# Optimization experiments

Measured on AMD Instinct MI355X. Metric: run time of the kernel, lower is better.

## Reference

```python
import jax, jax.numpy as jnp
import numpy as np
import math

D_MODEL = 2048
N_HEADS = 16
D_HEAD = D_MODEL // N_HEADS  # 128, also the RoPE dim
ROPE_BASE = 10000.0
B, T = 2, 2048


def _rope_cos_sin(seq_len, dim, dtype):
    inv_freq = 1.0 / (ROPE_BASE ** (jnp.arange(0, dim, 2, dtype=jnp.float32) / dim))
    t = jnp.arange(seq_len, dtype=jnp.float32)
    freqs = jnp.einsum('i,j->ij', t, inv_freq)          # [T, dim/2]
    emb = jnp.concatenate((freqs, freqs), axis=-1)       # [T, dim]  (half-concat layout, as in source)
    cos = jnp.cos(emb)[None, None, :, :].astype(dtype)   # [1,1,T,dim]
    sin = jnp.sin(emb)[None, None, :, :].astype(dtype)
    return cos, sin


def _apply_rot(x, cos, sin, dim):
    # interleaved pair rotation, faithful to the torch code
    x1 = x[..., 0:dim:2]
    x2 = x[..., 1:dim:2]
    x_rot = jnp.stack((-x2, x1), axis=-1).reshape(x.shape[:-1] + (dim,))
    return x[..., :dim] * cos + x_rot * sin


def setup_inputs() -> dict:
    key = jax.random.key(0)
    k1, k2, k3 = jax.random.split(key, 3)
    x = jax.random.normal(k1, (B, T, D_MODEL), dtype=jnp.float32)
    # causal additive mask, broadcastable to [B,H,T,T]
    neg = jnp.finfo(jnp.float32).min / 2
    causal = jnp.triu(jnp.full((T, T), neg, dtype=jnp.float32), k=1)
    mask = causal[None, None, :, :]
    Wqkv = jax.random.normal(k2, (D_MODEL, 3 * D_MODEL), dtype=jnp.float32) * (1.0 / math.sqrt(D_MODEL))
    bqkv = jnp.zeros((3 * D_MODEL,), dtype=jnp.float32)
    Wo = jax.random.normal(k3, (D_MODEL, D_MODEL), dtype=jnp.float32) * (1.0 / math.sqrt(D_MODEL))
    bo = jnp.zeros((D_MODEL,), dtype=jnp.float32)
    return {"x": x, "mask": mask, "Wqkv": Wqkv, "bqkv": bqkv, "Wo": Wo, "bo": bo}


def reference(x, mask, Wqkv, bqkv, Wo, bo):
    Bx, Tx, C = x.shape
    qkv = x @ Wqkv + bqkv                                     # [B,T,3C]
    qkv = qkv.reshape(Bx, Tx, 3, N_HEADS, D_HEAD)
    qkv = jnp.transpose(qkv, (2, 0, 3, 1, 4))                 # [3,B,H,T,dh]
    q, k, v = qkv[0], qkv[1], qkv[2]
    cos, sin = _rope_cos_sin(Tx, D_HEAD, x.dtype)
    q = _apply_rot(q, cos, sin, D_HEAD)
    k = _apply_rot(k, cos, sin, D_HEAD)
    att = jnp.einsum('bhqd,bhkd->bhqk', q, k) / math.sqrt(D_HEAD)
    att = att + mask
    att = jax.nn.softmax(att, axis=-1)
    y = jnp.einsum('bhqk,bhkd->bhqd', att, v)                 # [B,H,T,dh]
    y = jnp.transpose(y, (0, 2, 1, 3)).reshape(Bx, Tx, C)
    return y @ Wo + bo
```

## Files before the change

kernel.cpp:

```cpp
#include <hip/hip_runtime.h>
#include <stdint.h>

#define TDIM 2048
#define DMODEL 2048
#define NHEADS 16
#define DHEAD 128
#define NBATCH 2
#define NTOK (NBATCH * TDIM)
#define NQKV (3 * DMODEL)
#define BHTOT (NBATCH * NHEADS)

typedef unsigned short u16;
typedef __attribute__((ext_vector_type(8))) short bf16x8;
typedef __attribute__((ext_vector_type(4))) float f32x4;
typedef __attribute__((ext_vector_type(4))) int i32x4;

__device__ __forceinline__ u16 f2bf(float f) {
  union { float f; uint32_t u; } v; v.f = f;
  uint32_t u = v.u + 0x7fffu + ((v.u >> 16) & 1u);
  return (u16)(u >> 16);
}
__device__ __forceinline__ float bf2f(u16 h) {
  union { uint32_t u; float f; } v; v.u = ((uint32_t)h) << 16;
  return v.f;
}

#define GLOAD16(g, l)                                                        \
  __builtin_amdgcn_global_load_lds(                                          \
      (const __attribute__((address_space(1))) void*)(g),                    \
      (__attribute__((address_space(3))) void*)(l), 16, 0, 0)

__global__ void rope_table_kernel(float* __restrict__ ct, float* __restrict__ st) {
  int idx = blockIdx.x * 256 + threadIdx.x;
  int t = idx >> 6, m = idx & 63;
  float inv = expf(-(float)m * (9.210340371976184f / 64.0f));
  float ang = (float)t * inv;
  ct[idx] = cosf(ang);
  st[idx] = sinf(ang);
}

__global__ void convert_kernel(const float* __restrict__ in, u16* __restrict__ out) {
  int i = blockIdx.x * 256 + threadIdx.x;
  float4 v = ((const float4*)in)[i];
  ushort4 o;
  o.x = f2bf(v.x); o.y = f2bf(v.y); o.z = f2bf(v.z); o.w = f2bf(v.w);
  ((ushort4*)out)[i] = o;
}

__global__ __launch_bounds__(256) void transpose_convert_kernel(
    const float* __restrict__ in, u16* __restrict__ out, int K, int N) {
  __shared__ u16 tile[32][33];
  int n0 = blockIdx.x * 32, k0 = blockIdx.y * 32;
  int tx = threadIdx.x, ty = threadIdx.y;
  #pragma unroll
  for (int q = 0; q < 4; q++) {
    int k = ty + q * 8;
    tile[k][tx] = f2bf(in[(size_t)(k0 + k) * N + n0 + tx]);
  }
  __syncthreads();
  #pragma unroll
  for (int q = 0; q < 4; q++) {
    int n = ty + q * 8;
    out[(size_t)(n0 + n) * K + k0 + tx] = tile[tx][n];
  }
}

__global__ __launch_bounds__(256) void vtrans_kernel(
    const u16* __restrict__ Vtmp, u16* __restrict__ Vt) {
  __shared__ u16 tile[32][33];
  int bh = blockIdx.z;
  int t0 = blockIdx.x * 32, d0 = blockIdx.y * 32;
  int tx = threadIdx.x, ty = threadIdx.y;
  const u16* src = Vtmp + (size_t)bh * TDIM * DHEAD;
  u16* dst = Vt + (size_t)bh * DHEAD * TDIM;
  #pragma unroll
  for (int q = 0; q < 4; q++) {
    int t = ty + q * 8;
    tile[t][tx] = src[(size_t)(t0 + t) * DHEAD + d0 + tx];
  }
  __syncthreads();
  #pragma unroll
  for (int q = 0; q < 4; q++) {
    int d = ty + q * 8;
    dst[(size_t)(d0 + d) * TDIM + t0 + tx] = tile[tx][d];
  }
}

__global__ void rope_kernel(u16* __restrict__ X, const float* __restrict__ ct,
                            const float* __restrict__ st, float scale) {
  int idx = blockIdx.x * 256 + threadIdx.x;
  int i = idx & 63;
  int t = (idx >> 6) & (TDIM - 1);
  size_t base = (size_t)idx * 2;
  float x0 = bf2f(X[base]), x1 = bf2f(X[base + 1]);
  int j0 = (2 * i) & 63, j1 = (2 * i + 1) & 63;
  const float* ctt = ct + (size_t)t * 64;
  const float* stt = st + (size_t)t * 64;
  float c0 = ctt[j0], s0 = stt[j0], c1 = ctt[j1], s1 = stt[j1];
  X[base]     = f2bf((x0 * c0 - x1 * s0) * scale);
  X[base + 1] = f2bf((x1 * c1 + x0 * s1) * scale);
}

template <int MODE>
__global__ __launch_bounds__(512, 2) void gemm_bt_kernel(
    const u16* __restrict__ A, const u16* __restrict__ Bt,
    const float* __restrict__ bias,
    u16* __restrict__ q_out, u16* __restrict__ k_out, u16* __restrict__ v_out,
    float* __restrict__ f_out, int K) {
  __shared__ __attribute__((aligned(128))) char lds[2][49152];
  const int tid = threadIdx.x;
  const int lane = tid & 63, w = tid >> 6;
  const int wr = w >> 2, wc = w & 3;
  const int g = lane >> 4, c = lane & 15;
  const int m0 = blockIdx.x * 128, n0 = blockIdx.y * 256;
  const size_t rowb = (size_t)K * 2;
  const int NKT = K >> 6;

  const char* aSrc[2]; int aDst[2];
  const char* bSrc[4]; int bDst[4];
  #pragma unroll
  for (int p = 0; p < 2; p++) {
    int o = p * 8192 + tid * 16;
    int row = o >> 7, j = (o >> 4) & 7;
    aSrc[p] = (const char*)A + (size_t)(m0 + row) * rowb + ((j ^ (row & 7)) << 4);
    aDst[p] = o;
  }
  #pragma unroll
  for (int p = 0; p < 4; p++) {
    int o = p * 8192 + tid * 16;
    int row = o >> 7, j = (o >> 4) & 7;
    bSrc[p] = (const char*)Bt + (size_t)(n0 + row) * rowb + ((j ^ (row & 7)) << 4);
    bDst[p] = 16384 + o;
  }

#define STAGE(bufp, kt)                                                      \
  {                                                                          \
    const size_t kb_ = (size_t)(kt) * 128;                                   \
    _Pragma("unroll") for (int p_ = 0; p_ < 2; p_++)                         \
        GLOAD16(aSrc[p_] + kb_, (bufp) + aDst[p_]);                          \
    _Pragma("unroll") for (int p_ = 0; p_ < 4; p_++)                         \
        GLOAD16(bSrc[p_] + kb_, (bufp) + bDst[p_]);                          \
  }

  int aRd[4][2], bRd[4][2];
  #pragma unroll
  for (int m = 0; m < 4; m++) {
    #pragma unroll
    for (int ks = 0; ks < 2; ks++) {
      int arow = wr * 64 + m * 16 + c;
      aRd[m][ks] = arow * 128 + (((ks * 4 + g) ^ (c & 7)) << 4);
      int brow = wc * 64 + m * 16 + c;
      bRd[m][ks] = 16384 + brow * 128 + (((ks * 4 + g) ^ (c & 7)) << 4);
    }
  }

  const f32x4 zero = {0.f, 0.f, 0.f, 0.f};
  f32x4 acc[4][4];
  #pragma unroll
  for (int m = 0; m < 4; m++)
    #pragma unroll
    for (int n = 0; n < 4; n++) acc[m][n] = zero;

  STAGE(lds[0], 0);
  STAGE(lds[1], 1);
  asm volatile("s_waitcnt vmcnt(6)" ::: "memory");
  __builtin_amdgcn_s_barrier();
  __builtin_amdgcn_sched_barrier(0);

  int cur = 0;
  for (int kt = 0; kt < NKT; kt++) {
    char* bp = cur ? lds[1] : lds[0];
    bf16x8 bfr[4][2], afr[2][2], af2[2][2];
    #pragma unroll
    for (int n = 0; n < 4; n++)
      #pragma unroll
      for (int ks = 0; ks < 2; ks++)
        bfr[n][ks] = *(const bf16x8*)(bp + bRd[n][ks]);
    #pragma unroll
    for (int m = 0; m < 2; m++)
      #pragma unroll
      for (int ks = 0; ks < 2; ks++)
        afr[m][ks] = *(const bf16x8*)(bp + aRd[m][ks]);
    __builtin_amdgcn_s_setprio(1);
    #pragma unroll
    for (int ks = 0; ks < 2; ks++)
      #pragma unroll
      for (int m = 0; m < 2; m++)
        #pragma unroll
        for (int n = 0; n < 4; n++)
          acc[m][n] = __builtin_amdgcn_mfma_f32_16x16x32_bf16(
              afr[m][ks], bfr[n][ks], acc[m][n], 0, 0, 0);
    __builtin_amdgcn_s_setprio(0);

    #pragma unroll
    for (int m = 0; m < 2; m++)
      #pragma unroll
      for (int ks = 0; ks < 2; ks++)
        af2[m][ks] = *(const bf16x8*)(bp + aRd[m + 2][ks]);
    asm volatile("s_waitcnt lgkmcnt(0)" ::: "memory");
    __builtin_amdgcn_s_barrier();
    __builtin_amdgcn_sched_barrier(0);
    if (kt + 2 < NKT) STAGE(bp, kt + 2);
    __builtin_amdgcn_s_setprio(1);
    #pragma unroll
    for (int ks = 0; ks < 2; ks++)
      #pragma unroll
      for (int m = 0; m < 2; m++)
        #pragma unroll
        for (int n = 0; n < 4; n++)
          acc[m + 2][n] = __builtin_amdgcn_mfma_f32_16x16x32_bf16(
              af2[m][ks], bfr[n][ks], acc[m + 2][n], 0, 0, 0);
    __builtin_amdgcn_s_setprio(0);

    if (kt < NKT - 1) {
      if (kt + 2 < NKT) {
        asm volatile("s_waitcnt vmcnt(6)" ::: "memory");
      } else {
        asm volatile("s_waitcnt vmcnt(0)" ::: "memory");
      }
      __builtin_amdgcn_s_barrier();
      __builtin_amdgcn_sched_barrier(0);
    }
    cur ^= 1;
  }
#undef STAGE

  #pragma unroll
  for (int m = 0; m < 4; m++) {
    #pragma unroll
    for (int n = 0; n < 4; n++) {
      int gcol = n0 + wc * 64 + n * 16 + c;
      float bv = bias[gcol];
      #pragma unroll
      for (int r = 0; r < 4; r++) {
        int grow = m0 + wr * 64 + m * 16 + g * 4 + r;
        float val = acc[m][n][r] + bv;
        if (MODE == 0) {
          int s = gcol >> 11;
          int rem = gcol & 2047;
          int h = rem >> 7, d = rem & 127;
          int b = grow >> 11, t = grow & (TDIM - 1);
          size_t off = (((size_t)(b * NHEADS + h)) * TDIM + t) * DHEAD + d;
          u16 hv = f2bf(val);
          if (s == 0) q_out[off] = hv;
          else if (s == 1) k_out[off] = hv;
          else v_out[off] = hv;
        } else {
          f_out[(size_t)grow * DMODEL + gcol] = val;
        }
      }
    }
  }
}

__global__ __launch_bounds__(256) void attn_kernel(
    const u16* __restrict__ Q, const u16* __restrict__ K,
    const u16* __restrict__ Vt, u16* __restrict__ Yattn) {
  __shared__ u16 Ks[2][64 * 128];
  __shared__ u16 Vs[2][128 * 64];
  __shared__ u16 Ps[4][16 * 64];
  const int tid = threadIdx.x, lane = tid & 63, w = tid >> 6;
  const int g = lane >> 4, c = lane & 15;
  const int bh = blockIdx.y, b = bh >> 4, h = bh & 15;
  const u16* Qp = Q + (size_t)bh * TDIM * DHEAD;
  const u16* Kp = K + (size_t)bh * TDIM * DHEAD;
  const u16* Vp = Vt + (size_t)bh * DHEAD * TDIM;
  const f32x4 zero = {0.f, 0.f, 0.f, 0.f};

  for (int half = 0; half < 2; half++) {
    const int qt = half ? (31 - (int)blockIdx.x) : (int)blockIdx.x;
    const int qb = qt * 64 + w * 16;

    bf16x8 qf[4];
    #pragma unroll
    for (int kc = 0; kc < 4; kc++)
      qf[kc] = *(const bf16x8*)(Qp + (size_t)(qb + c) * DHEAD + kc * 32 + g * 8);

    f32x4 po[8];
    #pragma unroll
    for (int df = 0; df < 8; df++) po[df] = zero;
    float mrun[4], lrun[4];
    #pragma unroll
    for (int r = 0; r < 4; r++) { mrun[r] = -1e30f; lrun[r] = 0.f; }

    const int nt = qt + 1;

    {
      #pragma unroll
      for (int p = 0; p < 4; p++) {
        int off = p * 4096 + tid * 16;
        int kr = off >> 8, kc4 = (off & 255) >> 4;
        GLOAD16((const char*)Kp + (size_t)kr * 256 + ((kc4 ^ (kr & 7)) << 4),
                (char*)Ks[0] + off);
        int vr = off >> 7, vc4 = (off & 127) >> 4;
        GLOAD16((const char*)Vp + (size_t)vr * (TDIM * 2) + ((vc4 ^ (vr & 7)) << 4),
                (char*)Vs[0] + off);
      }
    }
    __syncthreads();

    int cur = 0;
    for (int t = 0; t < nt; t++) {
      if (t + 1 < nt) {
        int kv0n = (t + 1) * 64;
        char* KsN = (char*)Ks[cur ^ 1];
        char* VsN = (char*)Vs[cur ^ 1];
        #pragma unroll
        for (int p = 0; p < 4; p++) {
          int off = p * 4096 + tid * 16;
          int kr = off >> 8, kc4 = (off & 255) >> 4;
          GLOAD16((const char*)Kp + (size_t)(kv0n + kr) * 256 +
                      ((kc4 ^ (kr & 7)) << 4),
                  KsN + off);
          int vr = off >> 7, vc4 = (off & 127) >> 4;
          GLOAD16((const char*)Vp + (size_t)vr * (TDIM * 2) + (size_t)kv0n * 2 +
                      ((vc4 ^ (vr & 7)) << 4),
                  VsN + off);
        }
      }

      const u16* KsC = Ks[cur];
      const u16* VsC = Vs[cur];
      const int kv0 = t * 64;

      f32x4 sa[4];
      #pragma unroll
      for (int n = 0; n < 4; n++) sa[n] = zero;
      __builtin_amdgcn_s_setprio(1);
      #pragma unroll
      for (int n = 0; n < 4; n++) {
        int krow = n * 16 + c;
        #pragma unroll
        for (int kc = 0; kc < 4; kc++) {
          int kb = (kc * 32 + g * 8) * 2;
          bf16x8 kf = *(const bf16x8*)((const char*)KsC + krow * 256 +
                                       (kb ^ ((krow & 7) << 4)));
          sa[n] = __builtin_amdgcn_mfma_f32_16x16x32_bf16(qf[kc], kf, sa[n], 0, 0, 0);
        }
      }
      __builtin_amdgcn_s_setprio(0);

      if (kv0 + 63 > qb) {
        #pragma unroll
        for (int n = 0; n < 4; n++) {
          int col = kv0 + n * 16 + c;
          #pragma unroll
          for (int r = 0; r < 4; r++) {
            int qrow = qb + g * 4 + r;
            if (col > qrow) sa[n][r] = -1e30f;
          }
        }
      }

      float pvals[4][4];
      #pragma unroll
      for (int r = 0; r < 4; r++) {
        float vmax = fmaxf(fmaxf(sa[0][r], sa[1][r]), fmaxf(sa[2][r], sa[3][r]));
        #pragma unroll
        for (int d = 1; d < 16; d <<= 1) vmax = fmaxf(vmax, __shfl_xor(vmax, d, 64));
        float mnew = fmaxf(mrun[r], vmax);
        float scale = __expf(mrun[r] - mnew);
        float rs = 0.f;
        #pragma unroll
        for (int n = 0; n < 4; n++) {
          float p = __expf(sa[n][r] - mnew);
          pvals[r][n] = p;
          rs += p;
        }
        #pragma unroll
        for (int d = 1; d < 16; d <<= 1) rs += __shfl_xor(rs, d, 64);
        lrun[r] = lrun[r] * scale + rs;
        mrun[r] = mnew;
        #pragma unroll
        for (int df = 0; df < 8; df++) po[df][r] *= scale;
      }

      char* Pw = (char*)&Ps[w][0];
      #pragma unroll
      for (int r = 0; r < 4; r++) {
        int ri = g * 4 + r;
        #pragma unroll
        for (int n = 0; n < 4; n++) {
          int colb = (n * 16 + c) * 2;
          *(u16*)(Pw + ri * 128 + (colb ^ ((ri & 7) << 4))) = f2bf(pvals[r][n]);
        }
      }
      bf16x8 pa[2];
      #pragma unroll
      for (int kc2 = 0; kc2 < 2; kc2++) {
        int pb = (kc2 * 32 + g * 8) * 2;
        pa[kc2] = *(const bf16x8*)(Pw + c * 128 + (pb ^ ((c & 7) << 4)));
      }
      __builtin_amdgcn_s_setprio(1);
      #pragma unroll
      for (int df = 0; df < 8; df++) {
        #pragma unroll
        for (int kc2 = 0; kc2 < 2; kc2++) {
          int vrow = df * 16 + c;
          int vb = (kc2 * 32 + g * 8) * 2;
          bf16x8 vf = *(const bf16x8*)((const char*)VsC + vrow * 128 +
                                       (vb ^ ((vrow & 7) << 4)));
          po[df] = __builtin_amdgcn_mfma_f32_16x16x32_bf16(pa[kc2], vf, po[df], 0, 0, 0);
        }
      }
      __builtin_amdgcn_s_setprio(0);

      __syncthreads();
      cur ^= 1;
    }

    float inv[4];
    #pragma unroll
    for (int r = 0; r < 4; r++) inv[r] = 1.0f / lrun[r];
    #pragma unroll
    for (int df = 0; df < 8; df++) {
      #pragma unroll
      for (int r = 0; r < 4; r++) {
        int trow = qb + g * 4 + r;
        int col = h * DHEAD + df * 16 + c;
        Yattn[((size_t)b * TDIM + trow) * DMODEL + col] = f2bf(po[df][r] * inv[r]);
      }
    }
  }
}

extern "C" void kernel_launch(void* const* d_in, const int* in_sizes, int n_in,
                              void* d_out, int out_size, void* d_ws, size_t ws_size,
                              hipStream_t stream) {
  const float* x    = (const float*)d_in[0];
  const float* Wqkv = (const float*)d_in[2];
  const float* bqkv = (const float*)d_in[3];
  const float* Wo   = (const float*)d_in[4];
  const float* bo   = (const float*)d_in[5];
  float* out = (float*)d_out;

  char* ws = (char*)d_ws;
  size_t o = 0;
  u16* xb    = (u16*)(ws + o); o += (size_t)NTOK * DMODEL * 2;
  u16* Wqkvt = (u16*)(ws + o); o += (size_t)NQKV * DMODEL * 2;
  u16* Wot   = (u16*)(ws + o); o += (size_t)DMODEL * DMODEL * 2;
  u16* Qb    = (u16*)(ws + o); o += (size_t)BHTOT * TDIM * DHEAD * 2;
  u16* Kb    = (u16*)(ws + o); o += (size_t)BHTOT * TDIM * DHEAD * 2;
  u16* Vtmp  = (u16*)(ws + o); o += (size_t)BHTOT * TDIM * DHEAD * 2;
  float* ct  = (float*)(ws + o); o += (size_t)TDIM * 64 * 4;
  float* st  = (float*)(ws + o); o += (size_t)TDIM * 64 * 4;
  u16* Vt    = xb;
  u16* Yattn = Vtmp;

  dim3 tb32x8(32, 8);

  rope_table_kernel<<<(TDIM * 64) / 256, 256, 0, stream>>>(ct, st);
  convert_kernel<<<(NTOK * DMODEL / 4) / 256, 256, 0, stream>>>(x, xb);
  transpose_convert_kernel<<<dim3(NQKV / 32, DMODEL / 32), tb32x8, 0, stream>>>(
      Wqkv, Wqkvt, DMODEL, NQKV);
  transpose_convert_kernel<<<dim3(DMODEL / 32, DMODEL / 32), tb32x8, 0, stream>>>(
      Wo, Wot, DMODEL, DMODEL);

  gemm_bt_kernel<0><<<dim3(NTOK / 128, NQKV / 256), 512, 0, stream>>>(
      xb, Wqkvt, bqkv, Qb, Kb, Vtmp, nullptr, DMODEL);

  rope_kernel<<<(BHTOT * TDIM * 64) / 256, 256, 0, stream>>>(
      Qb, ct, st, 0.08838834764831845f);
  rope_kernel<<<(BHTOT * TDIM * 64) / 256, 256, 0, stream>>>(Kb, ct, st, 1.0f);

  vtrans_kernel<<<dim3(TDIM / 32, DHEAD / 32, BHTOT), tb32x8, 0, stream>>>(Vtmp, Vt);

  attn_kernel<<<dim3(16, BHTOT), 256, 0, stream>>>(Qb, Kb, Vt, Yattn);

  gemm_bt_kernel<1><<<dim3(NTOK / 128, DMODEL / 256), 512, 0, stream>>>(
      Yattn, Wot, bo, nullptr, nullptr, nullptr, out, DMODEL);
}
```

Before: 305.6 us.

## Fuse RoPE into QKV GEMM epilogue and switch to triple-buffered LDS pipeline

Removes the two standalone RoPE kernels by applying the rotation and the Q scaling in the QKV GEMM epilogue, with a lane shuffle supplying each pair's partner value. This avoids an extra read and write of Q and K. The GEMM main loop also moves from a double-buffered, split-phase schedule to a three-stage LDS ring with one barrier per k-step. That raises LDS per block to 144KB, which likely limits occupancy to one block per CU despite the launch bounds of 2.

```diff
diff --git a/kernel.cpp b/kernel.cpp
--- a/kernel.cpp
+++ b/kernel.cpp
@@ -86,28 +86,14 @@
   }
 }
 
-__global__ void rope_kernel(u16* __restrict__ X, const float* __restrict__ ct,
-                            const float* __restrict__ st, float scale) {
-  int idx = blockIdx.x * 256 + threadIdx.x;
-  int i = idx & 63;
-  int t = (idx >> 6) & (TDIM - 1);
-  size_t base = (size_t)idx * 2;
-  float x0 = bf2f(X[base]), x1 = bf2f(X[base + 1]);
-  int j0 = (2 * i) & 63, j1 = (2 * i + 1) & 63;
-  const float* ctt = ct + (size_t)t * 64;
-  const float* stt = st + (size_t)t * 64;
-  float c0 = ctt[j0], s0 = stt[j0], c1 = ctt[j1], s1 = stt[j1];
-  X[base]     = f2bf((x0 * c0 - x1 * s0) * scale);
-  X[base + 1] = f2bf((x1 * c1 + x0 * s1) * scale);
-}
-
 template <int MODE>
 __global__ __launch_bounds__(512, 2) void gemm_bt_kernel(
     const u16* __restrict__ A, const u16* __restrict__ Bt,
     const float* __restrict__ bias,
     u16* __restrict__ q_out, u16* __restrict__ k_out, u16* __restrict__ v_out,
-    float* __restrict__ f_out, int K) {
-  __shared__ __attribute__((aligned(128))) char lds[2][49152];
+    float* __restrict__ f_out,
+    const float* __restrict__ ct, const float* __restrict__ st, int K) {
+  __shared__ __attribute__((aligned(128))) char lds[3][49152];
   const int tid = threadIdx.x;
   const int lane = tid & 63, w = tid >> 6;
   const int wr = w >> 2, wc = w & 3;
@@ -163,65 +149,42 @@
 
   STAGE(lds[0], 0);
   STAGE(lds[1], 1);
-  asm volatile("s_waitcnt vmcnt(6)" ::: "memory");
-  __builtin_amdgcn_s_barrier();
-  __builtin_amdgcn_sched_barrier(0);
-
-  int cur = 0;
+
   for (int kt = 0; kt < NKT; kt++) {
-    char* bp = cur ? lds[1] : lds[0];
-    bf16x8 bfr[4][2], afr[2][2], af2[2][2];
+    if (kt + 1 < NKT) {
+      asm volatile("s_waitcnt vmcnt(6)" ::: "memory");
+    } else {
+      asm volatile("s_waitcnt vmcnt(0)" ::: "memory");
+    }
+    __builtin_amdgcn_s_barrier();
+    __builtin_amdgcn_sched_barrier(0);
+
+    char* bp = lds[kt % 3];
+    if (kt + 2 < NKT) STAGE(lds[(kt + 2) % 3], kt + 2);
+
+    bf16x8 afr[4][2], bfr[4][2];
     #pragma unroll
     for (int n = 0; n < 4; n++)
       #pragma unroll
       for (int ks = 0; ks < 2; ks++)
         bfr[n][ks] = *(const bf16x8*)(bp + bRd[n][ks]);
     #pragma unroll
-    for (int m = 0; m < 2; m++)
+    for (int m = 0; m < 4; m++)
       #pragma unroll
       for (int ks = 0; ks < 2; ks++)
         afr[m][ks] = *(const bf16x8*)(bp + aRd[m][ks]);
+
     __builtin_amdgcn_s_setprio(1);
     #pragma unroll
     for (int ks = 0; ks < 2; ks++)
       #pragma unroll
-      for (int m = 0; m < 2; m++)
+      for (int m = 0; m < 4; m++)
         #pragma unroll
         for (int n = 0; n < 4; n++)
           acc[m][n] = __builtin_amdgcn_mfma_f32_16x16x32_bf16(
               afr[m][ks], bfr[n][ks], acc[m][n], 0, 0, 0);
     __builtin_amdgcn_s_setprio(0);
-
-    #pragma unroll
-    for (int m = 0; m < 2; m++)
-      #pragma unroll
-      for (int ks = 0; ks < 2; ks++)
-        af2[m][ks] = *(const bf16x8*)(bp + aRd[m + 2][ks]);
-    asm volatile("s_waitcnt lgkmcnt(0)" ::: "memory");
-    __builtin_amdgcn_s_barrier();
     __builtin_amdgcn_sched_barrier(0);
-    if (kt + 2 < NKT) STAGE(bp, kt + 2);
-    __builtin_amdgcn_s_setprio(1);
-    #pragma unroll
-    for (int ks = 0; ks < 2; ks++)
-      #pragma unroll
-      for (int m = 0; m < 2; m++)
-        #pragma unroll
-        for (int n = 0; n < 4; n++)
-          acc[m + 2][n] = __builtin_amdgcn_mfma_f32_16x16x32_bf16(
-              af2[m][ks], bfr[n][ks], acc[m + 2][n], 0, 0, 0);
-    __builtin_amdgcn_s_setprio(0);
-
-    if (kt < NKT - 1) {
-      if (kt + 2 < NKT) {
-        asm volatile("s_waitcnt vmcnt(6)" ::: "memory");
-      } else {
-        asm volatile("s_waitcnt vmcnt(0)" ::: "memory");
-      }
-      __builtin_amdgcn_s_barrier();
-      __builtin_amdgcn_sched_barrier(0);
-    }
-    cur ^= 1;
   }
 #undef STAGE
 
@@ -231,22 +194,40 @@
     for (int n = 0; n < 4; n++) {
       int gcol = n0 + wc * 64 + n * 16 + c;
       float bv = bias[gcol];
-      #pragma unroll
-      for (int r = 0; r < 4; r++) {
-        int grow = m0 + wr * 64 + m * 16 + g * 4 + r;
-        float val = acc[m][n][r] + bv;
-        if (MODE == 0) {
-          int s = gcol >> 11;
-          int rem = gcol & 2047;
-          int h = rem >> 7, d = rem & 127;
-          int b = grow >> 11, t = grow & (TDIM - 1);
-          size_t off = (((size_t)(b * NHEADS + h)) * TDIM + t) * DHEAD + d;
-          u16 hv = f2bf(val);
-          if (s == 0) q_out[off] = hv;
-          else if (s == 1) k_out[off] = hv;
-          else v_out[off] = hv;
+      float val[4];
+      #pragma unroll
+      for (int r = 0; r < 4; r++) val[r] = acc[m][n][r] + bv;
+      if (MODE == 0) {
+        int s = n0 >> 11;
+        int rem = gcol & 2047;
+        int h = rem >> 7, d = rem & 127;
+        int b0 = (m0 + wr * 64 + m * 16) >> 11;
+        size_t hb = (((size_t)(b0 * NHEADS + h)) * TDIM) * DHEAD + d;
+        if (s == 2) {
+          #pragma unroll
+          for (int r = 0; r < 4; r++) {
+            int t = (m0 + wr * 64 + m * 16 + g * 4 + r) & (TDIM - 1);
+            v_out[hb + (size_t)t * DHEAD] = f2bf(val[r]);
+          }
         } else {
-          f_out[(size_t)grow * DMODEL + gcol] = val;
+          int mf = gcol & 63;
+          float sgn = (c & 1) ? 1.0f : -1.0f;
+          u16* dst = (s == 0) ? q_out : k_out;
+          float qs = (s == 0) ? 0.08838834764831845f : 1.0f;
+          #pragma unroll
+          for (int r = 0; r < 4; r++) {
+            float part = __shfl_xor(val[r], 1, 64);
+            int t = (m0 + wr * 64 + m * 16 + g * 4 + r) & (TDIM - 1);
+            float cs = ct[t * 64 + mf], sn = st[t * 64 + mf];
+            float rot = (val[r] * cs + sgn * part * sn) * qs;
+            dst[hb + (size_t)t * DHEAD] = f2bf(rot);
+          }
+        }
+      } else {
+        #pragma unroll
+        for (int r = 0; r < 4; r++) {
+          int grow = m0 + wr * 64 + m * 16 + g * 4 + r;
+          f_out[(size_t)grow * DMODEL + gcol] = val[r];
         }
       }
     }
@@ -457,16 +438,12 @@
       Wo, Wot, DMODEL, DMODEL);
 
   gemm_bt_kernel<0><<<dim3(NTOK / 128, NQKV / 256), 512, 0, stream>>>(
-      xb, Wqkvt, bqkv, Qb, Kb, Vtmp, nullptr, DMODEL);
-
-  rope_kernel<<<(BHTOT * TDIM * 64) / 256, 256, 0, stream>>>(
-      Qb, ct, st, 0.08838834764831845f);
-  rope_kernel<<<(BHTOT * TDIM * 64) / 256, 256, 0, stream>>>(Kb, ct, st, 1.0f);
+      xb, Wqkvt, bqkv, Qb, Kb, Vtmp, nullptr, ct, st, DMODEL);
 
   vtrans_kernel<<<dim3(TDIM / 32, DHEAD / 32, BHTOT), tb32x8, 0, stream>>>(Vtmp, Vt);
 
   attn_kernel<<<dim3(16, BHTOT), 256, 0, stream>>>(Qb, Kb, Vt, Yattn);
 
   gemm_bt_kernel<1><<<dim3(NTOK / 128, DMODEL / 256), 512, 0, stream>>>(
-      Yattn, Wot, bo, nullptr, nullptr, nullptr, out, DMODEL);
-}
+      Yattn, Wot, bo, nullptr, nullptr, nullptr, out, nullptr, nullptr, DMODEL);
+}
```

Result: faster. 294.1 us (-3.7%).
